# Kernel optimization log

Hardware: AMD Instinct MI355X
Metric: run time of the kernel (lower is better)

Reference implementation:

```python
import jax, jax.numpy as jnp
import numpy as np

B, S, D = 2, 2048, 1024
H, HD = 16, 64


def setup_inputs() -> dict:
    key = jax.random.key(0)
    ks = jax.random.split(key, 10)
    scale = 1.0 / np.sqrt(D)
    inputs_q = jax.random.normal(ks[0], (B, S, D), dtype=jnp.float32)
    inputs_kv = jax.random.normal(ks[1], (B, S, D), dtype=jnp.float32)
    # causal mask, broadcast over batch: True = attend
    mask = jnp.broadcast_to(jnp.tril(jnp.ones((S, S), dtype=bool)), (B, S, S))
    Wq = jax.random.normal(ks[2], (D, H * HD), dtype=jnp.float32) * scale
    bq = jnp.zeros((H * HD,), dtype=jnp.float32)
    Wk = jax.random.normal(ks[3], (D, H * HD), dtype=jnp.float32) * scale
    bk = jnp.zeros((H * HD,), dtype=jnp.float32)
    Wv = jax.random.normal(ks[4], (D, H * HD), dtype=jnp.float32) * scale
    bv = jnp.zeros((H * HD,), dtype=jnp.float32)
    Wo = jax.random.normal(ks[5], (H * HD, D), dtype=jnp.float32) * scale
    bo = jnp.zeros((D,), dtype=jnp.float32)
    return {"inputs_q": inputs_q, "inputs_kv": inputs_kv, "mask": mask,
            "Wq": Wq, "bq": bq, "Wk": Wk, "bk": bk, "Wv": Wv, "bv": bv,
            "Wo": Wo, "bo": bo}


def reference(inputs_q, inputs_kv, mask, Wq, bq, Wk, bk, Wv, bv, Wo, bo):
    b, s_q, _ = inputs_q.shape
    s_k = inputs_kv.shape[1]
    # projections -> [B, S, H, HD]
    q = (inputs_q @ Wq + bq).reshape(b, s_q, H, HD)
    k = (inputs_kv @ Wk + bk).reshape(b, s_k, H, HD)
    v = (inputs_kv @ Wv + bv).reshape(b, s_k, H, HD)
    q = q / jnp.sqrt(jnp.asarray(HD, dtype=q.dtype))
    # scores: [B, H, Sq, Sk]
    attn = jnp.einsum('bqhd,bkhd->bhqk', q, k)
    m = mask[:, None, :, :]  # [B,1,Sq,Sk] broadcast over heads
    attn = jnp.where(m, attn, jnp.asarray(-1e30, dtype=attn.dtype))
    attn = jax.nn.softmax(attn, axis=-1)
    # dropout_rate = 0.0, deterministic -> identity
    out = jnp.einsum('bhqk,bkhd->bqhd', attn, v).reshape(b, s_q, H * HD)
    return out @ Wo + bo
```

## Files before the change

kernel.cpp:

```cpp
#include <hip/hip_runtime.h>

typedef __attribute__((ext_vector_type(4))) float f32x4;
typedef __attribute__((ext_vector_type(8))) short bf16x8;
typedef unsigned short u16;
typedef unsigned int u32;

#define AS1 __attribute__((address_space(1)))
#define AS3 __attribute__((address_space(3)))

#define WAITVM(N) do{ asm volatile("s_waitcnt vmcnt(" #N ")" ::: "memory"); \
                      __builtin_amdgcn_sched_barrier(0); }while(0)
#define RAWBAR    do{ __builtin_amdgcn_s_barrier();                          \
                      __builtin_amdgcn_sched_barrier(0); }while(0)

__device__ __forceinline__ float fast_exp2(float x){
  return __builtin_amdgcn_exp2f(x);
}

__device__ __forceinline__ u16 f2bf(float x){
  u32 u = __float_as_uint(x);
  u += 0x7fffu + ((u >> 16) & 1u);
  return (u16)(u >> 16);
}
__device__ __forceinline__ u16 f2bf_fast(float x){
  return (u16)((__float_as_uint(x) + 0x8000u) >> 16);
}
__device__ __forceinline__ float bf2f(u16 x){
  return __uint_as_float((u32)x << 16);
}

__global__ __launch_bounds__(256) void prep(const float* __restrict__ W0,
                                            const float* __restrict__ W1,
                                            const float* __restrict__ W2,
                                            const float* __restrict__ W3,
                                            u16* __restrict__ Wt,
                                            const float* __restrict__ inq,
                                            const float* __restrict__ inkv,
                                            u16* __restrict__ Xq,
                                            u16* __restrict__ Xkv)
{
  const int z = blockIdx.z;
  if (z < 4){
    __shared__ float tile[32][33];
    const float* src = z == 0 ? W0 : z == 1 ? W1 : z == 2 ? W2 : W3;
    u16* d = Wt + (size_t)z * 1024 * 1024;
    int tx = threadIdx.x & 31, ty = threadIdx.x >> 5;
    int k0 = blockIdx.x * 32, n0 = blockIdx.y * 32;
    for (int r = 0; r < 4; ++r)
      tile[ty + r * 8][tx] = src[(size_t)(k0 + ty + r * 8) * 1024 + n0 + tx];
    __syncthreads();
    for (int r = 0; r < 4; ++r)
      d[(size_t)(n0 + ty + r * 8) * 1024 + k0 + tx] = f2bf(tile[tx][ty + r * 8]);
  } else {
    const float* src = z == 4 ? inq : inkv;
    u16* dst = z == 4 ? Xq : Xkv;
    int bid = blockIdx.y * 32 + blockIdx.x;
    size_t base4 = ((size_t)bid * 256 + threadIdx.x) * 4;
#pragma unroll
    for (int i = 0; i < 4; ++i){
      float4 v = reinterpret_cast<const float4*>(src)[base4 + i];
      ushort4 o;
      o.x = f2bf(v.x); o.y = f2bf(v.y); o.z = f2bf(v.z); o.w = f2bf(v.w);
      reinterpret_cast<ushort4*>(dst)[base4 + i] = o;
    }
  }
}

__global__ __launch_bounds__(512, 2) void gemm_qkv(const u16* __restrict__ Xq,
                                                   const u16* __restrict__ Xkv,
                                                   const u16* __restrict__ Wt,
                                                   const float* __restrict__ bq,
                                                   const float* __restrict__ bk,
                                                   const float* __restrict__ bv,
                                                   u16* __restrict__ Qb,
                                                   u16* __restrict__ Kb,
                                                   u16* __restrict__ Vt,
                                                   int M, int K)
{
  __shared__ u16 lA[3][256 * 32];
  __shared__ u16 lB[3][256 * 32];
  const int tid = threadIdx.x;
  const int l = tid & 63, w = tid >> 6;
  const int wr = w >> 2, wc = w & 3;
  const int bm0 = blockIdx.x * 256, bn0 = blockIdx.y * 256;
  const int seg = bn0 >> 10;
  const int nloc0 = bn0 & 1023;
  const u16* A = seg ? Xkv : Xq;
  const float* bias = seg == 0 ? bq : seg == 1 ? bk : bv;
  const float scale = seg == 0 ? 0.125f * 1.44269504089f : 1.0f;
  const int lr = l & 15, g4 = l >> 4;

#define STAGE_A(BI, KK) do{                                                   \
  _Pragma("unroll") for (int c_ = 0; c_ < 2; ++c_){                           \
    int e_ = c_ * 512 + tid;                                                  \
    int row_ = e_ >> 2, ch_ = e_ & 3;                                         \
    int sc_ = (ch_ ^ (row_ & 3)) * 8;                                         \
    __builtin_amdgcn_global_load_lds(                                         \
        (const AS1 u32*)(A + (size_t)(bm0 + row_) * K + (KK) * 32 + sc_),     \
        (AS3 u32*)(&lA[BI][e_ * 8]), 16, 0, 0);                               \
  }                                                                           \
}while(0)
#define STAGE_B(BI, KK) do{                                                   \
  _Pragma("unroll") for (int c_ = 0; c_ < 2; ++c_){                           \
    int e_ = c_ * 512 + tid;                                                  \
    int row_ = e_ >> 2, ch_ = e_ & 3;                                         \
    int sc_ = (ch_ ^ (row_ & 3)) * 8;                                         \
    __builtin_amdgcn_global_load_lds(                                         \
        (const AS1 u32*)(Wt + (size_t)(bn0 + row_) * K + (KK) * 32 + sc_),    \
        (AS3 u32*)(&lB[BI][e_ * 8]), 16, 0, 0);                               \
  }                                                                           \
}while(0)

#define RD(LDS, ROW) (*reinterpret_cast<const bf16x8*>(                       \
    reinterpret_cast<const char*>(LDS) + (ROW) * 64 + ((g4 ^ ((ROW) & 3)) << 4)))

  f32x4 acc[8][4];
#pragma unroll
  for (int m = 0; m < 8; ++m)
#pragma unroll
    for (int n = 0; n < 4; ++n) acc[m][n] = (f32x4){0.f, 0.f, 0.f, 0.f};

  STAGE_A(0, 0); STAGE_B(0, 0);
  STAGE_A(1, 1); STAGE_B(1, 1);

#pragma unroll
  for (int k = 0; k < 32; ++k){
    const int cur = k % 3;
    if (k < 30){ STAGE_A((k + 2) % 3, k + 2); WAITVM(6); }
    else if (k == 30){ WAITVM(4); }
    else { WAITVM(0); }
    RAWBAR;

    bf16x8 aLo[4], bF[4];
#pragma unroll
    for (int m = 0; m < 4; ++m)
      aLo[m] = RD(lA[cur], wr * 128 + m * 16 + lr);
#pragma unroll
    for (int n = 0; n < 4; ++n)
      bF[n] = RD(lB[cur], wc * 64 + n * 16 + lr);
    __builtin_amdgcn_s_setprio(1);
#pragma unroll
    for (int m = 0; m < 4; ++m)
#pragma unroll
      for (int n = 0; n < 4; ++n)
        acc[m][n] = __builtin_amdgcn_mfma_f32_16x16x32_bf16(aLo[m], bF[n], acc[m][n], 0, 0, 0);
    __builtin_amdgcn_s_setprio(0);
    RAWBAR;

    if (k < 30) STAGE_B((k + 2) % 3, k + 2);
    bf16x8 aHi[4];
#pragma unroll
    for (int m = 0; m < 4; ++m)
      aHi[m] = RD(lA[cur], wr * 128 + (m + 4) * 16 + lr);
    __builtin_amdgcn_s_setprio(1);
#pragma unroll
    for (int m = 0; m < 4; ++m)
#pragma unroll
      for (int n = 0; n < 4; ++n)
        acc[m + 4][n] = __builtin_amdgcn_mfma_f32_16x16x32_bf16(aHi[m], bF[n], acc[m + 4][n], 0, 0, 0);
    __builtin_amdgcn_s_setprio(0);
    RAWBAR;
  }
#undef STAGE_A
#undef STAGE_B
#undef RD

  const int r0 = g4 * 4;
  if (seg < 2){
    u16* C = seg == 0 ? Qb : Kb;
#pragma unroll
    for (int m = 0; m < 8; ++m)
#pragma unroll
      for (int n = 0; n < 4; ++n){
        int col = nloc0 + wc * 64 + n * 16 + lr;
        float bv_ = bias[col];
#pragma unroll
        for (int r = 0; r < 4; ++r){
          int row = bm0 + wr * 128 + m * 16 + r0 + r;
          C[(size_t)row * 1024 + col] = f2bf((acc[m][n][r] + bv_) * scale);
        }
      }
  } else {
#pragma unroll
    for (int m = 0; m < 8; ++m)
#pragma unroll
      for (int n = 0; n < 4; ++n){
        int col = nloc0 + wc * 64 + n * 16 + lr;
        float bv_ = bias[col];
        int h = col >> 6, hdl = col & 63;
#pragma unroll
        for (int r = 0; r < 4; ++r){
          int row = bm0 + wr * 128 + m * 16 + r0 + r;
          int b = row >> 11, kv = row & 2047;
          size_t off = ((size_t)(b * 16 + h)) * 131072 + (size_t)hdl * 2048 + kv;
          Vt[off] = f2bf(acc[m][n][r] + bv_);
        }
      }
  }
}

__global__ __launch_bounds__(256) void gemm_out(const u16* __restrict__ A,
                                                const u16* __restrict__ Bt,
                                                const float* __restrict__ bias,
                                                float* __restrict__ Cf,
                                                int M, int N, int K)
{
  __shared__ u16 lA[3][64 * 32];
  __shared__ u16 lB[3][128 * 32];
  const int tid = threadIdx.x;
  const int l = tid & 63, w = tid >> 6;
  const int wr = w >> 1, wc = w & 1;
  const int bm0 = blockIdx.x * 64, bn0 = blockIdx.y * 128;
  const int lr = l & 15, lg = (l >> 4) * 8;

#define STAGE_O(BI, KK) do{                                                   \
  {                                                                           \
    int e_ = tid * 8;                                                         \
    int row_ = e_ >> 5, col_ = e_ & 31;                                       \
    __builtin_amdgcn_global_load_lds(                                         \
        (const AS1 u32*)(A + (size_t)(bm0 + row_) * K + (KK) * 32 + col_),    \
        (AS3 u32*)(&lA[BI][e_]), 16, 0, 0);                                   \
  }                                                                           \
  _Pragma("unroll") for (int c_ = 0; c_ < 2; ++c_){                           \
    int e_ = (c_ * 256 + tid) * 8;                                            \
    int row_ = e_ >> 5, col_ = e_ & 31;                                       \
    __builtin_amdgcn_global_load_lds(                                         \
        (const AS1 u32*)(Bt + (size_t)(bn0 + row_) * K + (KK) * 32 + col_),   \
        (AS3 u32*)(&lB[BI][e_]), 16, 0, 0);                                   \
  }                                                                           \
}while(0)

  f32x4 acc[2][4];
#pragma unroll
  for (int m = 0; m < 2; ++m)
#pragma unroll
    for (int n = 0; n < 4; ++n) acc[m][n] = (f32x4){0.f, 0.f, 0.f, 0.f};

  STAGE_O(0, 0);
  STAGE_O(1, 1);

#pragma unroll
  for (int k = 0; k < 32; ++k){
    const int cur = k % 3;
    if (k < 30){ STAGE_O((k + 2) % 3, k + 2); WAITVM(6); }
    else if (k == 30){ WAITVM(3); }
    else { WAITVM(0); }
    RAWBAR;

    bf16x8 aF[2], bF[4];
#pragma unroll
    for (int m = 0; m < 2; ++m)
      aF[m] = *reinterpret_cast<const bf16x8*>(&lA[cur][(wr * 32 + m * 16 + lr) * 32 + lg]);
#pragma unroll
    for (int n = 0; n < 4; ++n)
      bF[n] = *reinterpret_cast<const bf16x8*>(&lB[cur][(wc * 64 + n * 16 + lr) * 32 + lg]);
    __builtin_amdgcn_s_setprio(1);
#pragma unroll
    for (int m = 0; m < 2; ++m)
#pragma unroll
      for (int n = 0; n < 4; ++n)
        acc[m][n] = __builtin_amdgcn_mfma_f32_16x16x32_bf16(aF[m], bF[n], acc[m][n], 0, 0, 0);
    __builtin_amdgcn_s_setprio(0);
    RAWBAR;
  }
#undef STAGE_O

  const int r0 = (l >> 4) * 4;
#pragma unroll
  for (int m = 0; m < 2; ++m)
#pragma unroll
    for (int n = 0; n < 4; ++n){
      int col = bn0 + wc * 64 + n * 16 + lr;
      float bv_ = bias[col];
#pragma unroll
      for (int r = 0; r < 4; ++r){
        int row = bm0 + wr * 32 + m * 16 + r0 + r;
        Cf[(size_t)row * N + col] = acc[m][n][r] + bv_;
      }
    }
}

__global__ __launch_bounds__(512, 2) void attn_fwd(const u16* __restrict__ Qb,
                                                   const u16* __restrict__ Kb,
                                                   const u16* __restrict__ Vt,
                                                   u16* __restrict__ Po,
                                                   float* __restrict__ Pl, int S)
{
  __shared__ u16 lK[2][64 * 64];
  __shared__ u16 lV[2][64 * 64];
  __shared__ u16 lP[8][16 * 72];
  const int tid = threadIdx.x, l = tid & 63, w = tid >> 6;
  const int j = blockIdx.x;
  const int jj = j & 255;
  const int xcd = jj & 7;
  const int bh = xcd * 4 + ((jj >> 3) & 3);
  const int p = jj >> 5;
  const int rnd = j >> 8;
  const int qt = (rnd & 1) ? (15 - p) : p;
  const int half = rnd >> 1;
  const int t0 = half ? (qt + 1) : 0;
  const int t1 = (qt + 1) << half ? (half ? (2 * qt + 2) : (qt + 1)) : (qt + 1);
  const int bb = bh >> 4;
  const size_t baseQK = ((size_t)bb * S) * 1024 + (bh & 15) * 64;
  const u16* gK = Kb + baseQK;
  const u16* gV = Vt + (size_t)bh * 131072;
  const int lr = l & 15, g4 = l >> 4, lg = g4 * 8;

  u16* lPw = (u16*)lP[w];
  bf16x8 ones;
#pragma unroll
  for (int i = 0; i < 8; ++i) ones[i] = (short)0x3F80;

#define STAGE_KV(T, BI) do{                                                   \
  int row_ = tid >> 3, ch_ = tid & 7, sc_ = (ch_ ^ (row_ & 7)) * 8;           \
  __builtin_amdgcn_global_load_lds(                                           \
      (const AS1 u32*)(gK + (size_t)(64 * (T) + row_) * 1024 + sc_),          \
      (AS3 u32*)(&lK[BI][tid * 8]), 16, 0, 0);                                \
  __builtin_amdgcn_global_load_lds(                                           \
      (const AS1 u32*)(gV + (size_t)row_ * 2048 + 64 * (T) + sc_),            \
      (AS3 u32*)(&lV[BI][tid * 8]), 16, 0, 0);                                \
}while(0)

  const int q0 = qt * 128 + w * 16;

  bf16x8 qf[2];
#pragma unroll
  for (int kc = 0; kc < 2; ++kc)
    qf[kc] = *reinterpret_cast<const bf16x8*>(
        Qb + baseQK + (size_t)(q0 + lr) * 1024 + kc * 32 + lg);

  f32x4 acc_o[4], acc_l;
  acc_l = (f32x4){0.f, 0.f, 0.f, 0.f};
#pragma unroll
  for (int n = 0; n < 4; ++n) acc_o[n] = (f32x4){0.f, 0.f, 0.f, 0.f};

  int buf = 0;
  STAGE_KV(t0, 0);
  for (int t = t0; t < t1; ++t){
    if (t + 1 < t1){ STAGE_KV(t + 1, buf ^ 1); WAITVM(2); }
    else           { WAITVM(0); }
    RAWBAR;

    if (64 * t <= q0 + 15){
      const u16* lKb = lK[buf];
      const u16* lVb = lV[buf];
      f32x4 sA[4];
#pragma unroll
      for (int np = 0; np < 4; ++np) sA[np] = (f32x4){0.f, 0.f, 0.f, 0.f};
      __builtin_amdgcn_s_setprio(1);
#pragma unroll
      for (int kc = 0; kc < 2; ++kc)
#pragma unroll
        for (int np = 0; np < 4; ++np){
          int row = np * 16 + lr, ch = kc * 4 + g4;
          bf16x8 kf = *reinterpret_cast<const bf16x8*>(
              reinterpret_cast<const char*>(lKb) + row * 128 + ((ch ^ (row & 7)) << 4));
          sA[np] = __builtin_amdgcn_mfma_f32_16x16x32_bf16(qf[kc], kf, sA[np], 0, 0, 0);
        }
      __builtin_amdgcn_s_setprio(0);

      const bool needmask = (64 * t + 63 > q0);
      if (needmask){
#pragma unroll
        for (int np = 0; np < 4; ++np){
          int kvg = 64 * t + np * 16 + lr;
#pragma unroll
          for (int r = 0; r < 4; ++r){
            int qg = q0 + g4 * 4 + r;
            float e = fast_exp2(sA[np][r]);
            lPw[(g4 * 4 + r) * 72 + np * 16 + lr] = f2bf_fast((kvg <= qg) ? e : 0.f);
          }
        }
      } else {
#pragma unroll
        for (int np = 0; np < 4; ++np)
#pragma unroll
          for (int r = 0; r < 4; ++r)
            lPw[(g4 * 4 + r) * 72 + np * 16 + lr] = f2bf_fast(fast_exp2(sA[np][r]));
      }

      bf16x8 pf[2];
#pragma unroll
      for (int kc = 0; kc < 2; ++kc)
        pf[kc] = *reinterpret_cast<const bf16x8*>(
            reinterpret_cast<const char*>(lPw) + lr * 144 + (kc * 4 + g4) * 16);
      __builtin_amdgcn_s_setprio(1);
#pragma unroll
      for (int kc = 0; kc < 2; ++kc){
        acc_l = __builtin_amdgcn_mfma_f32_16x16x32_bf16(pf[kc], ones, acc_l, 0, 0, 0);
#pragma unroll
        for (int n = 0; n < 4; ++n){
          int row = n * 16 + lr, ch = kc * 4 + g4;
          bf16x8 vf = *reinterpret_cast<const bf16x8*>(
              reinterpret_cast<const char*>(lVb) + row * 128 + ((ch ^ (row & 7)) << 4));
          acc_o[n] = __builtin_amdgcn_mfma_f32_16x16x32_bf16(pf[kc], vf, acc_o[n], 0, 0, 0);
        }
      }
      __builtin_amdgcn_s_setprio(0);
    }
    RAWBAR;
    buf ^= 1;
  }

  const int part = (bh * 16 + qt) * 2 + half;
  u16* po = Po + (size_t)part * 8192;
  float* pl = Pl + part * 128;
#pragma unroll
  for (int n = 0; n < 4; ++n)
#pragma unroll
    for (int r = 0; r < 4; ++r){
      int rl = w * 16 + g4 * 4 + r;
      po[rl * 64 + n * 16 + lr] = f2bf(acc_o[n][r]);
    }
  if (lr == 0){
#pragma unroll
    for (int r = 0; r < 4; ++r)
      pl[w * 16 + g4 * 4 + r] = acc_l[r];
  }
#undef STAGE_KV
}

__global__ __launch_bounds__(256) void attn_combine(const u16* __restrict__ Po,
                                                    const float* __restrict__ Pl,
                                                    u16* __restrict__ AO, int S)
{
  const int g = blockIdx.x;
  const int bh = g >> 4, qt = g & 15;
  const int bb = bh >> 4, h = bh & 15;
  const size_t base = ((size_t)bb * S) * 1024 + h * 64;
  const u16* o0 = Po + (size_t)(g * 2 + 0) * 8192;
  const u16* o1 = Po + (size_t)(g * 2 + 1) * 8192;
  const float* l0 = Pl + (g * 2 + 0) * 128;
  const float* l1 = Pl + (g * 2 + 1) * 128;
  const int cg = (threadIdx.x & 15) * 4, rb = threadIdx.x >> 4;
#pragma unroll
  for (int r = 0; r < 8; ++r){
    int row = rb * 8 + r;
    float inv = 1.0f / (l0[row] + l1[row]);
    ushort4 a = *reinterpret_cast<const ushort4*>(&o0[row * 64 + cg]);
    ushort4 b = *reinterpret_cast<const ushort4*>(&o1[row * 64 + cg]);
    ushort4 o;
    o.x = f2bf((bf2f(a.x) + bf2f(b.x)) * inv);
    o.y = f2bf((bf2f(a.y) + bf2f(b.y)) * inv);
    o.z = f2bf((bf2f(a.z) + bf2f(b.z)) * inv);
    o.w = f2bf((bf2f(a.w) + bf2f(b.w)) * inv);
    *reinterpret_cast<ushort4*>(&AO[base + (size_t)(qt * 128 + row) * 1024 + cg]) = o;
  }
}

extern "C" void kernel_launch(void* const* d_in, const int* in_sizes, int n_in,
                              void* d_out, int out_size, void* d_ws, size_t ws_size,
                              hipStream_t stream)
{
  const float* inq  = (const float*)d_in[0];
  const float* inkv = (const float*)d_in[1];
  const float* Wq = (const float*)d_in[3];
  const float* bq = (const float*)d_in[4];
  const float* Wk = (const float*)d_in[5];
  const float* bk = (const float*)d_in[6];
  const float* Wv = (const float*)d_in[7];
  const float* bv = (const float*)d_in[8];
  const float* Wo = (const float*)d_in[9];
  const float* bo = (const float*)d_in[10];
  float* out = (float*)d_out;

  const int B = 2, S = 2048, D = 1024;
  const int M = B * S;

  char* ws = (char*)d_ws;
  const size_t MB = 1024ull * 1024ull;
  u16* Xq  = (u16*)(ws + 0 * MB);
  u16* Po  = (u16*)(ws + 0 * MB);
  u16* Xkv = (u16*)(ws + 8 * MB);
  u16* Wt  = (u16*)(ws + 16 * MB);
  float* Pl = (float*)(ws + 16 * MB);
  u16* Wot = (u16*)(ws + 22 * MB);
  u16* Qb  = (u16*)(ws + 24 * MB);
  u16* Kb  = (u16*)(ws + 32 * MB);
  u16* Vtg = (u16*)(ws + 40 * MB);
  u16* AOb = (u16*)(ws + 48 * MB);

  prep<<<dim3(32, 32, 6), 256, 0, stream>>>(Wq, Wk, Wv, Wo, Wt, inq, inkv, Xq, Xkv);

  gemm_qkv<<<dim3(M / 256, 3072 / 256), 512, 0, stream>>>(Xq, Xkv, Wt, bq, bk, bv,
                                                          Qb, Kb, Vtg, M, D);

  attn_fwd<<<dim3(1024), 512, 0, stream>>>(Qb, Kb, Vtg, Po, Pl, S);

  attn_combine<<<dim3(512), 256, 0, stream>>>(Po, Pl, AOb, S);

  gemm_out<<<dim3(M / 64, D / 128), 256, 0, stream>>>(AOb, Wot, bo, out, M, D, D);
}
```

Baseline: 118.2 us.

## Fuse split-KV attention combine into output projection GEMM prologue

Removes the separate attn_combine kernel and its AO intermediate buffer. The output-projection GEMM now loads both partial attention outputs directly from Po, sums them and scales by the reciprocal of the summed softmax denominators while building A fragments in registers. This saves one launch and a full write and read of the combined activation. In exchange each GEMM block (8 blocks per row tile along N) redundantly reads twice the A data and redoes the combine arithmetic, which adds VALU work in the MFMA loop. The t1 expression is also simplified to an equivalent form.

```diff
diff --git a/kernel.cpp b/kernel.cpp
--- a/kernel.cpp
+++ b/kernel.cpp
@@ -199,87 +199,6 @@
   }
 }
 
-__global__ __launch_bounds__(256) void gemm_out(const u16* __restrict__ A,
-                                                const u16* __restrict__ Bt,
-                                                const float* __restrict__ bias,
-                                                float* __restrict__ Cf,
-                                                int M, int N, int K)
-{
-  __shared__ u16 lA[3][64 * 32];
-  __shared__ u16 lB[3][128 * 32];
-  const int tid = threadIdx.x;
-  const int l = tid & 63, w = tid >> 6;
-  const int wr = w >> 1, wc = w & 1;
-  const int bm0 = blockIdx.x * 64, bn0 = blockIdx.y * 128;
-  const int lr = l & 15, lg = (l >> 4) * 8;
-
-#define STAGE_O(BI, KK) do{                                                   \
-  {                                                                           \
-    int e_ = tid * 8;                                                         \
-    int row_ = e_ >> 5, col_ = e_ & 31;                                       \
-    __builtin_amdgcn_global_load_lds(                                         \
-        (const AS1 u32*)(A + (size_t)(bm0 + row_) * K + (KK) * 32 + col_),    \
-        (AS3 u32*)(&lA[BI][e_]), 16, 0, 0);                                   \
-  }                                                                           \
-  _Pragma("unroll") for (int c_ = 0; c_ < 2; ++c_){                           \
-    int e_ = (c_ * 256 + tid) * 8;                                            \
-    int row_ = e_ >> 5, col_ = e_ & 31;                                       \
-    __builtin_amdgcn_global_load_lds(                                         \
-        (const AS1 u32*)(Bt + (size_t)(bn0 + row_) * K + (KK) * 32 + col_),   \
-        (AS3 u32*)(&lB[BI][e_]), 16, 0, 0);                                   \
-  }                                                                           \
-}while(0)
-
-  f32x4 acc[2][4];
-#pragma unroll
-  for (int m = 0; m < 2; ++m)
-#pragma unroll
-    for (int n = 0; n < 4; ++n) acc[m][n] = (f32x4){0.f, 0.f, 0.f, 0.f};
-
-  STAGE_O(0, 0);
-  STAGE_O(1, 1);
-
-#pragma unroll
-  for (int k = 0; k < 32; ++k){
-    const int cur = k % 3;
-    if (k < 30){ STAGE_O((k + 2) % 3, k + 2); WAITVM(6); }
-    else if (k == 30){ WAITVM(3); }
-    else { WAITVM(0); }
-    RAWBAR;
-
-    bf16x8 aF[2], bF[4];
-#pragma unroll
-    for (int m = 0; m < 2; ++m)
-      aF[m] = *reinterpret_cast<const bf16x8*>(&lA[cur][(wr * 32 + m * 16 + lr) * 32 + lg]);
-#pragma unroll
-    for (int n = 0; n < 4; ++n)
-      bF[n] = *reinterpret_cast<const bf16x8*>(&lB[cur][(wc * 64 + n * 16 + lr) * 32 + lg]);
-    __builtin_amdgcn_s_setprio(1);
-#pragma unroll
-    for (int m = 0; m < 2; ++m)
-#pragma unroll
-      for (int n = 0; n < 4; ++n)
-        acc[m][n] = __builtin_amdgcn_mfma_f32_16x16x32_bf16(aF[m], bF[n], acc[m][n], 0, 0, 0);
-    __builtin_amdgcn_s_setprio(0);
-    RAWBAR;
-  }
-#undef STAGE_O
-
-  const int r0 = (l >> 4) * 4;
-#pragma unroll
-  for (int m = 0; m < 2; ++m)
-#pragma unroll
-    for (int n = 0; n < 4; ++n){
-      int col = bn0 + wc * 64 + n * 16 + lr;
-      float bv_ = bias[col];
-#pragma unroll
-      for (int r = 0; r < 4; ++r){
-        int row = bm0 + wr * 32 + m * 16 + r0 + r;
-        Cf[(size_t)row * N + col] = acc[m][n][r] + bv_;
-      }
-    }
-}
-
 __global__ __launch_bounds__(512, 2) void attn_fwd(const u16* __restrict__ Qb,
                                                    const u16* __restrict__ Kb,
                                                    const u16* __restrict__ Vt,
@@ -299,7 +218,7 @@
   const int qt = (rnd & 1) ? (15 - p) : p;
   const int half = rnd >> 1;
   const int t0 = half ? (qt + 1) : 0;
-  const int t1 = (qt + 1) << half ? (half ? (2 * qt + 2) : (qt + 1)) : (qt + 1);
+  const int t1 = half ? (2 * qt + 2) : (qt + 1);
   const int bb = bh >> 4;
   const size_t baseQK = ((size_t)bb * S) * 1024 + (bh & 15) * 64;
   const u16* gK = Kb + baseQK;
@@ -420,32 +339,113 @@
 #undef STAGE_KV
 }
 
-__global__ __launch_bounds__(256) void attn_combine(const u16* __restrict__ Po,
-                                                    const float* __restrict__ Pl,
-                                                    u16* __restrict__ AO, int S)
+__global__ __launch_bounds__(256) void gemm_out(const u16* __restrict__ Po,
+                                                const float* __restrict__ Pl,
+                                                const u16* __restrict__ Bt,
+                                                const float* __restrict__ bias,
+                                                float* __restrict__ Cf,
+                                                int M, int N, int K)
 {
-  const int g = blockIdx.x;
-  const int bh = g >> 4, qt = g & 15;
-  const int bb = bh >> 4, h = bh & 15;
-  const size_t base = ((size_t)bb * S) * 1024 + h * 64;
-  const u16* o0 = Po + (size_t)(g * 2 + 0) * 8192;
-  const u16* o1 = Po + (size_t)(g * 2 + 1) * 8192;
-  const float* l0 = Pl + (g * 2 + 0) * 128;
-  const float* l1 = Pl + (g * 2 + 1) * 128;
-  const int cg = (threadIdx.x & 15) * 4, rb = threadIdx.x >> 4;
-#pragma unroll
-  for (int r = 0; r < 8; ++r){
-    int row = rb * 8 + r;
-    float inv = 1.0f / (l0[row] + l1[row]);
-    ushort4 a = *reinterpret_cast<const ushort4*>(&o0[row * 64 + cg]);
-    ushort4 b = *reinterpret_cast<const ushort4*>(&o1[row * 64 + cg]);
-    ushort4 o;
-    o.x = f2bf((bf2f(a.x) + bf2f(b.x)) * inv);
-    o.y = f2bf((bf2f(a.y) + bf2f(b.y)) * inv);
-    o.z = f2bf((bf2f(a.z) + bf2f(b.z)) * inv);
-    o.w = f2bf((bf2f(a.w) + bf2f(b.w)) * inv);
-    *reinterpret_cast<ushort4*>(&AO[base + (size_t)(qt * 128 + row) * 1024 + cg]) = o;
-  }
+  __shared__ u16 lA[3][2][64 * 32];
+  __shared__ u16 lB[3][128 * 32];
+  const int tid = threadIdx.x;
+  const int l = tid & 63, w = tid >> 6;
+  const int wr = w >> 1, wc = w & 1;
+  const int bm0 = blockIdx.x * 64, bn0 = blockIdx.y * 128;
+  const int lr = l & 15, lg = (l >> 4) * 8;
+  const int bb = bm0 >> 11;
+  const int qt = (bm0 & 2047) >> 7;
+  const int rl0 = bm0 & 127;
+
+  float inv_l[16][2];
+#pragma unroll
+  for (int h = 0; h < 16; ++h){
+    int pbase = (((bb * 16 + h) * 16 + qt) * 2) * 128;
+#pragma unroll
+    for (int m = 0; m < 2; ++m){
+      int rA = rl0 + wr * 32 + m * 16 + lr;
+      float l0 = Pl[pbase + rA];
+      float l1 = Pl[pbase + 128 + rA];
+      inv_l[h][m] = 1.0f / (l0 + l1);
+    }
+  }
+
+#define STAGE_O(BI, KK) do{                                                   \
+  const int h_ = (KK) >> 1, hd0_ = ((KK) & 1) * 32;                           \
+  const size_t pb_ = (size_t)(((bb * 16 + h_) * 16 + qt) * 2) * 8192;         \
+  {                                                                           \
+    int row_ = tid >> 2, ch_ = tid & 3;                                       \
+    __builtin_amdgcn_global_load_lds(                                         \
+        (const AS1 u32*)(Po + pb_ + (size_t)(rl0 + row_) * 64 + hd0_ + ch_ * 8), \
+        (AS3 u32*)(&lA[BI][0][tid * 8]), 16, 0, 0);                           \
+    __builtin_amdgcn_global_load_lds(                                         \
+        (const AS1 u32*)(Po + pb_ + 8192 + (size_t)(rl0 + row_) * 64 + hd0_ + ch_ * 8), \
+        (AS3 u32*)(&lA[BI][1][tid * 8]), 16, 0, 0);                           \
+  }                                                                           \
+  _Pragma("unroll") for (int c_ = 0; c_ < 2; ++c_){                           \
+    int e_ = (c_ * 256 + tid) * 8;                                            \
+    int row_ = e_ >> 5, col_ = e_ & 31;                                       \
+    __builtin_amdgcn_global_load_lds(                                         \
+        (const AS1 u32*)(Bt + (size_t)(bn0 + row_) * K + (KK) * 32 + col_),   \
+        (AS3 u32*)(&lB[BI][e_]), 16, 0, 0);                                   \
+  }                                                                           \
+}while(0)
+
+  f32x4 acc[2][4];
+#pragma unroll
+  for (int m = 0; m < 2; ++m)
+#pragma unroll
+    for (int n = 0; n < 4; ++n) acc[m][n] = (f32x4){0.f, 0.f, 0.f, 0.f};
+
+  STAGE_O(0, 0);
+  STAGE_O(1, 1);
+
+#pragma unroll
+  for (int k = 0; k < 32; ++k){
+    const int cur = k % 3;
+    if (k < 30){ STAGE_O((k + 2) % 3, k + 2); WAITVM(8); }
+    else if (k == 30){ WAITVM(4); }
+    else { WAITVM(0); }
+    RAWBAR;
+
+    bf16x8 aF[2], bF[4];
+#pragma unroll
+    for (int m = 0; m < 2; ++m){
+      int ro = (wr * 32 + m * 16 + lr) * 32 + lg;
+      bf16x8 a0 = *reinterpret_cast<const bf16x8*>(&lA[cur][0][ro]);
+      bf16x8 a1 = *reinterpret_cast<const bf16x8*>(&lA[cur][1][ro]);
+      float s = inv_l[k >> 1][m];
+#pragma unroll
+      for (int i = 0; i < 8; ++i)
+        aF[m][i] = (short)f2bf_fast((bf2f((u16)a0[i]) + bf2f((u16)a1[i])) * s);
+    }
+#pragma unroll
+    for (int n = 0; n < 4; ++n)
+      bF[n] = *reinterpret_cast<const bf16x8*>(&lB[cur][(wc * 64 + n * 16 + lr) * 32 + lg]);
+    __builtin_amdgcn_s_setprio(1);
+#pragma unroll
+    for (int m = 0; m < 2; ++m)
+#pragma unroll
+      for (int n = 0; n < 4; ++n)
+        acc[m][n] = __builtin_amdgcn_mfma_f32_16x16x32_bf16(aF[m], bF[n], acc[m][n], 0, 0, 0);
+    __builtin_amdgcn_s_setprio(0);
+    RAWBAR;
+  }
+#undef STAGE_O
+
+  const int r0 = (l >> 4) * 4;
+#pragma unroll
+  for (int m = 0; m < 2; ++m)
+#pragma unroll
+    for (int n = 0; n < 4; ++n){
+      int col = bn0 + wc * 64 + n * 16 + lr;
+      float bv_ = bias[col];
+#pragma unroll
+      for (int r = 0; r < 4; ++r){
+        int row = bm0 + wr * 32 + m * 16 + r0 + r;
+        Cf[(size_t)row * N + col] = acc[m][n][r] + bv_;
+      }
+    }
 }
 
 extern "C" void kernel_launch(void* const* d_in, const int* in_sizes, int n_in,
@@ -478,7 +478,6 @@
   u16* Qb  = (u16*)(ws + 24 * MB);
   u16* Kb  = (u16*)(ws + 32 * MB);
   u16* Vtg = (u16*)(ws + 40 * MB);
-  u16* AOb = (u16*)(ws + 48 * MB);
 
   prep<<<dim3(32, 32, 6), 256, 0, stream>>>(Wq, Wk, Wv, Wo, Wt, inq, inkv, Xq, Xkv);
 
@@ -487,7 +486,5 @@
 
   attn_fwd<<<dim3(1024), 512, 0, stream>>>(Qb, Kb, Vtg, Po, Pl, S);
 
-  attn_combine<<<dim3(512), 256, 0, stream>>>(Po, Pl, AOb, S);
-
-  gemm_out<<<dim3(M / 64, D / 128), 256, 0, stream>>>(AOb, Wot, bo, out, M, D, D);
-}
+  gemm_out<<<dim3(M / 64, D / 128), 256, 0, stream>>>(Po, Pl, Wot, bo, out, M, D, D);
+}
```

Measured after the change: 121.4 us. +2.7%, slower.
